# Kernel optimization log

Hardware: AMD Instinct MI355X
Metric: run time of the kernel (lower is better)

## Reference

```python
import jax, jax.numpy as jnp
import numpy as np

D_MODEL = 1024
N_HEAD = 16
D_K = D_MODEL // N_HEAD


def setup_inputs() -> dict:
    key = jax.random.key(0)
    ks = jax.random.split(key, 7)
    B, S = 4, 2048
    scale = 1.0 / np.sqrt(D_MODEL)
    x = jax.random.normal(ks[0], (B, S, D_MODEL), dtype=jnp.float32)
    Wq = jax.random.normal(ks[1], (D_MODEL, D_MODEL), dtype=jnp.float32) * scale
    Wk = jax.random.normal(ks[2], (D_MODEL, D_MODEL), dtype=jnp.float32) * scale
    Wv = jax.random.normal(ks[3], (D_MODEL, D_MODEL), dtype=jnp.float32) * scale
    bq = jax.random.normal(ks[4], (D_MODEL,), dtype=jnp.float32) * 0.01
    bk = jax.random.normal(ks[5], (D_MODEL,), dtype=jnp.float32) * 0.01
    bv = jax.random.normal(ks[6], (D_MODEL,), dtype=jnp.float32) * 0.01
    return {"x": x, "Wq": Wq, "bq": bq, "Wk": Wk, "bk": bk, "Wv": Wv, "bv": bv}


def reference(x, Wq, bq, Wk, bk, Wv, bv):
    B, S, _ = x.shape
    # QKV projections (nn.Linear: x @ W.T + b; weights here stored as [in, out])
    Q = x @ Wq + bq  # [B, S, D]
    K = x @ Wk + bk
    V = x @ Wv + bv
    # split heads -> [B, H, S, d_k]
    def split(t):
        return t.reshape(B, S, N_HEAD, D_K).transpose(0, 2, 1, 3)
    Qh, Kh, Vh = split(Q), split(K), split(V)
    scores = jnp.einsum('bhqd,bhkd->bhqk', Qh, Kh) / jnp.sqrt(jnp.float32(D_K))
    attn = jax.nn.softmax(scores, axis=-1)
    ctx = jnp.einsum('bhqk,bhkd->bhqd', attn, Vh)  # [B, H, S, d_k]
    return ctx.transpose(0, 2, 1, 3).reshape(B, S, D_MODEL)
```

## Files before the change

### kernel.cpp

```cpp
#include <hip/hip_runtime.h>
#include <stdint.h>

#define D_MODEL 1024
#define NHEAD   16
#define DK      64
#define BATCH   4
#define SEQ     2048
#define MTOT    (BATCH*SEQ)
#define KVB     64
#define NT      (SEQ/KVB)

typedef __attribute__((ext_vector_type(4)))  float  f32x4;
typedef __attribute__((ext_vector_type(16))) float  f32x16;
typedef __attribute__((ext_vector_type(8)))  __bf16 bf16x8;
typedef __attribute__((ext_vector_type(8)))  unsigned short u16x8;
typedef __attribute__((ext_vector_type(4)))  unsigned int u32x4;

#define QSCALE 0.1803368801111244f

__device__ __forceinline__ unsigned short f2bf(float f) {
    unsigned u = __builtin_bit_cast(unsigned, f);
    u += 0x7fffu + ((u >> 16) & 1u);
    return (unsigned short)(u >> 16);
}

__global__ __launch_bounds__(256) void cvt_x_kernel(const float* __restrict__ x,
                                                    unsigned short* __restrict__ xb) {
    size_t i = ((size_t)blockIdx.x * 256 + threadIdx.x) * 8;
    f32x4 a = *(const f32x4*)(x + i);
    f32x4 b = *(const f32x4*)(x + i + 4);
    u16x8 o;
    o[0] = f2bf(a[0]); o[1] = f2bf(a[1]); o[2] = f2bf(a[2]); o[3] = f2bf(a[3]);
    o[4] = f2bf(b[0]); o[5] = f2bf(b[1]); o[6] = f2bf(b[2]); o[7] = f2bf(b[3]);
    *(u16x8*)(xb + i) = o;
}

__global__ __launch_bounds__(256) void cvt_wt_kernel(const float* __restrict__ Wq,
                                                     const float* __restrict__ Wk,
                                                     const float* __restrict__ Wv,
                                                     unsigned short* __restrict__ wt) {
    __shared__ float tile[32][33];
    int mat = blockIdx.z;
    const float* W = (mat == 0) ? Wq : (mat == 1) ? Wk : Wv;
    int n0 = blockIdx.x * 32;
    int k0 = blockIdx.y * 32;
    int tx = threadIdx.x;
    int ty = threadIdx.y;
    #pragma unroll
    for (int i = 0; i < 4; ++i)
        tile[ty + i*8][tx] = W[(size_t)(k0 + ty + i*8) * D_MODEL + n0 + tx];
    __syncthreads();
    unsigned short* dst = wt + (size_t)mat * D_MODEL * D_MODEL;
    #pragma unroll
    for (int i = 0; i < 4; ++i)
        dst[(size_t)(n0 + ty + i*8) * D_MODEL + k0 + tx] = f2bf(tile[tx][ty + i*8]);
}

#define BM 128
#define BN 128
#define BKK 64
__global__ __launch_bounds__(256) void qkv_gemm_kernel(const unsigned short* __restrict__ xb,
                                                       const unsigned short* __restrict__ wt,
                                                       const float* __restrict__ bq,
                                                       const float* __restrict__ bk,
                                                       const float* __restrict__ bv,
                                                       unsigned short* __restrict__ qkv) {
    __shared__ __align__(16) unsigned char sA[BM * BKK * 2];
    __shared__ __align__(16) unsigned char sB[BN * BKK * 2];

    int nb   = blockIdx.x;
    int mb   = blockIdx.y;
    int mat  = nb >> 3;
    int col0 = (nb & 7) * BN;
    int m0   = mb * BM;
    int t    = threadIdx.x;
    int lane = t & 63;
    int w    = t >> 6;

    const unsigned short* wmat = wt + (size_t)mat * D_MODEL * D_MODEL;
    const float* bias = (mat == 0) ? bq : (mat == 1) ? bk : bv;

    f32x4 acc[4][4];
    #pragma unroll
    for (int i = 0; i < 4; ++i)
        #pragma unroll
        for (int j = 0; j < 4; ++j)
            acc[i][j] = (f32x4)0.0f;

    int rA = (w >> 1) * 64;
    int rB = (w & 1) * 64;

    for (int ks = 0; ks < D_MODEL / BKK; ++ks) {
        int K0 = ks * BKK;
        #pragma unroll
        for (int i = 0; i < 4; ++i) {
            int c   = t + 256 * i;
            int row = c >> 3;
            int kc  = c & 7;
            int swz = kc ^ (row & 7);
            const unsigned short* ga = xb + (size_t)(m0 + row) * D_MODEL + K0 + swz * 8;
            __builtin_amdgcn_global_load_lds(
                (const __attribute__((address_space(1))) void*)ga,
                (__attribute__((address_space(3))) void*)(sA + c * 16), 16, 0, 0);
            const unsigned short* gb = wmat + (size_t)(col0 + row) * D_MODEL + K0 + swz * 8;
            __builtin_amdgcn_global_load_lds(
                (const __attribute__((address_space(1))) void*)gb,
                (__attribute__((address_space(3))) void*)(sB + c * 16), 16, 0, 0);
        }
        __syncthreads();

        #pragma unroll
        for (int kk = 0; kk < 2; ++kk) {
            bf16x8 af[4], bf[4];
            int kc = kk * 4 + (lane >> 4);
            #pragma unroll
            for (int mt = 0; mt < 4; ++mt) {
                int row = rA + mt * 16 + (lane & 15);
                int swz = kc ^ (row & 7);
                af[mt] = *(const bf16x8*)(sA + row * 128 + swz * 16);
            }
            #pragma unroll
            for (int nt = 0; nt < 4; ++nt) {
                int row = rB + nt * 16 + (lane & 15);
                int swz = kc ^ (row & 7);
                bf[nt] = *(const bf16x8*)(sB + row * 128 + swz * 16);
            }
            #pragma unroll
            for (int mt = 0; mt < 4; ++mt)
                #pragma unroll
                for (int nt = 0; nt < 4; ++nt)
                    acc[mt][nt] = __builtin_amdgcn_mfma_f32_16x16x32_bf16(
                        af[mt], bf[nt], acc[mt][nt], 0, 0, 0);
        }
        __syncthreads();
    }

    #pragma unroll
    for (int mt = 0; mt < 4; ++mt) {
        #pragma unroll
        for (int nt = 0; nt < 4; ++nt) {
            int gn = col0 + rB + nt * 16 + (lane & 15);
            float bval = bias[gn];
            #pragma unroll
            for (int r = 0; r < 4; ++r) {
                int gm = m0 + rA + mt * 16 + (lane >> 4) * 4 + r;
                float v = acc[mt][nt][r] + bval;
                if (mat == 0) v *= QSCALE;
                int b = gm >> 11, s = gm & 2047;
                int h = gn >> 6,  d = gn & 63;
                size_t idx;
                if (mat == 2)
                    idx = ((size_t)(b * NHEAD + h) * DK + d) * SEQ + s;
                else
                    idx = ((size_t)(b * NHEAD + h) * SEQ + s) * DK + d;
                qkv[(size_t)mat * MTOT * D_MODEL + idx] = f2bf(v);
            }
        }
    }
}

#define CVTPK(dst, lo_, hi_) \
    asm("v_cvt_pk_bf16_f32 %0, %1, %2" : "=v"(dst) : "v"(lo_), "v"(hi_))
#define PLSWAP(x_, y_) \
    asm("v_permlane32_swap_b32 %0, %1" : "+v"(x_), "+v"(y_))
#define EXP2(dst, x_) \
    asm("v_exp_f32 %0, %1" : "=v"(dst) : "v"(x_))

__device__ __forceinline__ bf16x8 make_pf(float p0, float p1, float p2, float p3,
                                          float p4, float p5, float p6, float p7) {
    unsigned a1, a2, b1, b2;
    CVTPK(a1, p0, p1); CVTPK(a2, p2, p3);
    CVTPK(b1, p4, p5); CVTPK(b2, p6, p7);
    PLSWAP(a1, b1); PLSWAP(a2, b2);
    u32x4 u = { a1, a2, b1, b2 };
    return __builtin_bit_cast(bf16x8, u);
}

__device__ __forceinline__ float vmax16(const f32x16& v) {
    float a = fmaxf(fmaxf(v[0], v[1]),   fmaxf(v[2], v[3]));
    float b = fmaxf(fmaxf(v[4], v[5]),   fmaxf(v[6], v[7]));
    float c = fmaxf(fmaxf(v[8], v[9]),   fmaxf(v[10], v[11]));
    float d = fmaxf(fmaxf(v[12], v[13]), fmaxf(v[14], v[15]));
    return fmaxf(fmaxf(a, b), fmaxf(c, d));
}

__global__ __launch_bounds__(512, 2) void attn_kernel(const unsigned short* __restrict__ qkv,
                                                      float* __restrict__ out) {
    __shared__ __align__(16) unsigned char lds[32768];

    int bh = blockIdx.x;
    int qb = blockIdx.y;
    int t = threadIdx.x;
    int lane = t & 63;
    int w = t >> 6;
    int hi = lane >> 5;
    int l31 = lane & 31;

    const unsigned short* Qb = qkv + (size_t)bh * SEQ * DK;
    const unsigned short* Kb = qkv + (size_t)MTOT * D_MODEL + (size_t)bh * SEQ * DK;
    const unsigned short* Vt = qkv + (size_t)2 * MTOT * D_MODEL + (size_t)bh * DK * SEQ;

    int qbase = qb * 256 + w * 32;

    bf16x8 aq[4];
    #pragma unroll
    for (int kd = 0; kd < 4; ++kd)
        aq[kd] = *(const bf16x8*)(Qb + (size_t)(qbase + l31) * DK + kd * 16 + hi * 8);

    f32x16 o0 = (f32x16)0.0f, o1 = (f32x16)0.0f;
    float mrun = -3e38f, lrun = 0.0f;

#define STAGE(tile_, bo_) do {                                                         \
    int kv0_ = (tile_) * KVB;                                                          \
    int row_ = t >> 3, kc_ = t & 7;                                                    \
    int sw_ = (kc_ ^ (row_ & 7)) * 8;                                                  \
    __builtin_amdgcn_global_load_lds(                                                  \
        (const __attribute__((address_space(1))) void*)(Kb + (size_t)(kv0_ + row_) * DK + sw_), \
        (__attribute__((address_space(3))) void*)(lds + (bo_) + t * 16), 16, 0, 0);             \
    __builtin_amdgcn_global_load_lds(                                                  \
        (const __attribute__((address_space(1))) void*)(Vt + (size_t)row_ * SEQ + kv0_ + sw_),  \
        (__attribute__((address_space(3))) void*)(lds + 16384 + (bo_) + t * 16), 16, 0, 0);     \
} while (0)

    int swz7 = l31 & 7;
    int cofs0 = ((0 + hi) ^ swz7) << 4;
    int cofs1 = ((2 + hi) ^ swz7) << 4;
    int cofs2 = ((4 + hi) ^ swz7) << 4;
    int cofs3 = ((6 + hi) ^ swz7) << 4;

    STAGE(0, 0);
    __syncthreads();
    int buf = 0;

    for (int kt = 0; kt < NT; ++kt) {
        if (kt + 1 < NT)
            STAGE(kt + 1, (buf ^ 1) * 8192);

        const unsigned char* kb = lds + buf * 8192;
        const unsigned char* vb = lds + 16384 + buf * 8192;
        const unsigned char* kr0 = kb + l31 * 128;
        const unsigned char* kr1 = kb + (32 + l31) * 128;
        const unsigned char* vr0 = vb + l31 * 128;
        const unsigned char* vr1 = vb + (32 + l31) * 128;

        bf16x8 ak00 = *(const bf16x8*)(kr0 + cofs0);
        bf16x8 ak01 = *(const bf16x8*)(kr0 + cofs1);
        bf16x8 ak02 = *(const bf16x8*)(kr0 + cofs2);
        bf16x8 ak03 = *(const bf16x8*)(kr0 + cofs3);
        bf16x8 ak10 = *(const bf16x8*)(kr1 + cofs0);
        bf16x8 ak11 = *(const bf16x8*)(kr1 + cofs1);
        bf16x8 ak12 = *(const bf16x8*)(kr1 + cofs2);
        bf16x8 ak13 = *(const bf16x8*)(kr1 + cofs3);
        f32x16 sc0 = (f32x16)0.0f, sc1 = (f32x16)0.0f;
        __builtin_amdgcn_s_setprio(1);
        sc0 = __builtin_amdgcn_mfma_f32_32x32x16_bf16(ak00, aq[0], sc0, 0, 0, 0);
        sc1 = __builtin_amdgcn_mfma_f32_32x32x16_bf16(ak10, aq[0], sc1, 0, 0, 0);
        sc0 = __builtin_amdgcn_mfma_f32_32x32x16_bf16(ak01, aq[1], sc0, 0, 0, 0);
        sc1 = __builtin_amdgcn_mfma_f32_32x32x16_bf16(ak11, aq[1], sc1, 0, 0, 0);
        sc0 = __builtin_amdgcn_mfma_f32_32x32x16_bf16(ak02, aq[2], sc0, 0, 0, 0);
        sc1 = __builtin_amdgcn_mfma_f32_32x32x16_bf16(ak12, aq[2], sc1, 0, 0, 0);
        sc0 = __builtin_amdgcn_mfma_f32_32x32x16_bf16(ak03, aq[3], sc0, 0, 0, 0);
        sc1 = __builtin_amdgcn_mfma_f32_32x32x16_bf16(ak13, aq[3], sc1, 0, 0, 0);
        __builtin_amdgcn_s_setprio(0);

        bf16x8 av00 = *(const bf16x8*)(vr0 + cofs0);
        bf16x8 av01 = *(const bf16x8*)(vr0 + cofs1);
        bf16x8 av02 = *(const bf16x8*)(vr0 + cofs2);
        bf16x8 av03 = *(const bf16x8*)(vr0 + cofs3);
        bf16x8 av10 = *(const bf16x8*)(vr1 + cofs0);
        bf16x8 av11 = *(const bf16x8*)(vr1 + cofs1);
        bf16x8 av12 = *(const bf16x8*)(vr1 + cofs2);
        bf16x8 av13 = *(const bf16x8*)(vr1 + cofs3);

        float mx = fmaxf(vmax16(sc0), vmax16(sc1));
        mx = fmaxf(mx, __shfl_xor(mx, 32));
        if (!__all(mx <= mrun + 8.0f)) {
            float mnew = fmaxf(mrun, mx);
            float al;  EXP2(al, mrun - mnew);
            lrun *= al;
            #pragma unroll
            for (int i = 0; i < 16; ++i) { o0[i] *= al; o1[i] *= al; }
            mrun = mnew;
        }
        #pragma unroll
        for (int i = 0; i < 16; ++i) { float p; EXP2(p, sc0[i] - mrun); sc0[i] = p; }
        #pragma unroll
        for (int i = 0; i < 16; ++i) { float p; EXP2(p, sc1[i] - mrun); sc1[i] = p; }
        float r0 = 0.f, r1 = 0.f, r2 = 0.f, r3 = 0.f;
        #pragma unroll
        for (int i = 0; i < 4; ++i) {
            r0 += sc0[i] + sc1[i];     r1 += sc0[4+i] + sc1[4+i];
            r2 += sc0[8+i] + sc1[8+i]; r3 += sc0[12+i] + sc1[12+i];
        }
        float rs = (r0 + r1) + (r2 + r3);
        rs += __shfl_xor(rs, 32);
        lrun += rs;

        bf16x8 pf0 = make_pf(sc0[0], sc0[1], sc0[2],  sc0[3],  sc0[4],  sc0[5],  sc0[6],  sc0[7]);
        bf16x8 pf1 = make_pf(sc0[8], sc0[9], sc0[10], sc0[11], sc0[12], sc0[13], sc0[14], sc0[15]);
        bf16x8 pf2 = make_pf(sc1[0], sc1[1], sc1[2],  sc1[3],  sc1[4],  sc1[5],  sc1[6],  sc1[7]);
        bf16x8 pf3 = make_pf(sc1[8], sc1[9], sc1[10], sc1[11], sc1[12], sc1[13], sc1[14], sc1[15]);

        __builtin_amdgcn_s_setprio(1);
        o0 = __builtin_amdgcn_mfma_f32_32x32x16_bf16(av00, pf0, o0, 0, 0, 0);
        o1 = __builtin_amdgcn_mfma_f32_32x32x16_bf16(av10, pf0, o1, 0, 0, 0);
        o0 = __builtin_amdgcn_mfma_f32_32x32x16_bf16(av01, pf1, o0, 0, 0, 0);
        o1 = __builtin_amdgcn_mfma_f32_32x32x16_bf16(av11, pf1, o1, 0, 0, 0);
        o0 = __builtin_amdgcn_mfma_f32_32x32x16_bf16(av02, pf2, o0, 0, 0, 0);
        o1 = __builtin_amdgcn_mfma_f32_32x32x16_bf16(av12, pf2, o1, 0, 0, 0);
        o0 = __builtin_amdgcn_mfma_f32_32x32x16_bf16(av03, pf3, o0, 0, 0, 0);
        o1 = __builtin_amdgcn_mfma_f32_32x32x16_bf16(av13, pf3, o1, 0, 0, 0);
        __builtin_amdgcn_s_setprio(0);

        __syncthreads();
        buf ^= 1;
    }
#undef STAGE

    int b = bh >> 4, h = bh & 15;
    float rl = 1.0f / lrun;
    float* dst = out + ((size_t)b * SEQ + qbase + l31) * D_MODEL + h * DK;
    #pragma unroll
    for (int g = 0; g < 4; ++g) {
        int d0 = 8 * g + 4 * hi;
        f32x4 v0 = { o0[4*g] * rl, o0[4*g+1] * rl, o0[4*g+2] * rl, o0[4*g+3] * rl };
        *(f32x4*)(dst + d0) = v0;
        f32x4 v1 = { o1[4*g] * rl, o1[4*g+1] * rl, o1[4*g+2] * rl, o1[4*g+3] * rl };
        *(f32x4*)(dst + 32 + d0) = v1;
    }
}

extern "C" void kernel_launch(void* const* d_in, const int* in_sizes, int n_in,
                              void* d_out, int out_size, void* d_ws, size_t ws_size,
                              hipStream_t stream) {
    const float* x  = (const float*)d_in[0];
    const float* Wq = (const float*)d_in[1];
    const float* bq = (const float*)d_in[2];
    const float* Wk = (const float*)d_in[3];
    const float* bk = (const float*)d_in[4];
    const float* Wv = (const float*)d_in[5];
    const float* bv = (const float*)d_in[6];
    float* out = (float*)d_out;

    unsigned short* xb  = (unsigned short*)d_ws;
    unsigned short* wt  = xb + (size_t)MTOT * D_MODEL;
    unsigned short* qkv = wt + (size_t)3 * D_MODEL * D_MODEL;

    cvt_x_kernel<<<dim3(MTOT * D_MODEL / (256 * 8)), dim3(256), 0, stream>>>(x, xb);
    cvt_wt_kernel<<<dim3(32, 32, 3), dim3(32, 8), 0, stream>>>(Wq, Wk, Wv, wt);
    qkv_gemm_kernel<<<dim3(24, 64), dim3(256), 0, stream>>>(xb, wt, bq, bk, bv, qkv);
    attn_kernel<<<dim3(64, 8), dim3(512), 0, stream>>>(qkv, out);
}
```

Before: 201.0 us.

## Triple-buffer attention K/V staging, swizzle GEMM block order, reshape max tree

The attention kernel moves from double to triple buffering of K/V tiles in LDS (48KB). Each iteration prefetches two tiles ahead and waits with explicit vmcnt counts plus a raw barrier, so global load latency can overlap more compute. The QKV GEMM remaps its block index so consecutive blocks are spread across M rows, aiming at better L2 locality. The row-max reduction tree is also restructured. The cost is more LDS per block, which could limit occupancy at two blocks per CU, and the hand-written vmcnt waits are correctness-sensitive.

```diff
diff --git a/kernel.cpp b/kernel.cpp
--- a/kernel.cpp
+++ b/kernel.cpp
@@ -68,8 +68,10 @@
     __shared__ __align__(16) unsigned char sA[BM * BKK * 2];
     __shared__ __align__(16) unsigned char sB[BN * BKK * 2];
 
-    int nb   = blockIdx.x;
-    int mb   = blockIdx.y;
+    int lin = blockIdx.y * 24 + blockIdx.x;
+    lin = (lin & 7) * 192 + (lin >> 3);
+    int nb   = lin % 24;
+    int mb   = lin / 24;
     int mat  = nb >> 3;
     int col0 = (nb & 7) * BN;
     int m0   = mb * BM;
@@ -177,16 +179,18 @@
 }
 
 __device__ __forceinline__ float vmax16(const f32x16& v) {
-    float a = fmaxf(fmaxf(v[0], v[1]),   fmaxf(v[2], v[3]));
-    float b = fmaxf(fmaxf(v[4], v[5]),   fmaxf(v[6], v[7]));
-    float c = fmaxf(fmaxf(v[8], v[9]),   fmaxf(v[10], v[11]));
-    float d = fmaxf(fmaxf(v[12], v[13]), fmaxf(v[14], v[15]));
+    float a = fmaxf(fmaxf(v[0],  v[1]),  v[2]);
+    float b = fmaxf(fmaxf(v[3],  v[4]),  v[5]);
+    float c = fmaxf(fmaxf(v[6],  v[7]),  v[8]);
+    float d = fmaxf(fmaxf(v[9],  v[10]), v[11]);
+    a = fmaxf(fmaxf(a, v[12]), v[13]);
+    b = fmaxf(fmaxf(b, v[14]), v[15]);
     return fmaxf(fmaxf(a, b), fmaxf(c, d));
 }
 
 __global__ __launch_bounds__(512, 2) void attn_kernel(const unsigned short* __restrict__ qkv,
                                                       float* __restrict__ out) {
-    __shared__ __align__(16) unsigned char lds[32768];
+    __shared__ __align__(16) unsigned char lds[49152];
 
     int bh = blockIdx.x;
     int qb = blockIdx.y;
@@ -210,16 +214,16 @@
     f32x16 o0 = (f32x16)0.0f, o1 = (f32x16)0.0f;
     float mrun = -3e38f, lrun = 0.0f;
 
-#define STAGE(tile_, bo_) do {                                                         \
+#define STAGE(tile_, b_) do {                                                          \
     int kv0_ = (tile_) * KVB;                                                          \
     int row_ = t >> 3, kc_ = t & 7;                                                    \
     int sw_ = (kc_ ^ (row_ & 7)) * 8;                                                  \
     __builtin_amdgcn_global_load_lds(                                                  \
         (const __attribute__((address_space(1))) void*)(Kb + (size_t)(kv0_ + row_) * DK + sw_), \
-        (__attribute__((address_space(3))) void*)(lds + (bo_) + t * 16), 16, 0, 0);             \
+        (__attribute__((address_space(3))) void*)(lds + (b_) * 8192 + t * 16), 16, 0, 0);       \
     __builtin_amdgcn_global_load_lds(                                                  \
         (const __attribute__((address_space(1))) void*)(Vt + (size_t)row_ * SEQ + kv0_ + sw_),  \
-        (__attribute__((address_space(3))) void*)(lds + 16384 + (bo_) + t * 16), 16, 0, 0);     \
+        (__attribute__((address_space(3))) void*)(lds + 24576 + (b_) * 8192 + t * 16), 16, 0, 0); \
 } while (0)
 
     int swz7 = l31 & 7;
@@ -229,15 +233,18 @@
     int cofs3 = ((6 + hi) ^ swz7) << 4;
 
     STAGE(0, 0);
-    __syncthreads();
-    int buf = 0;
+    STAGE(1, 1);
+    asm volatile("s_waitcnt vmcnt(2)" ::: "memory");
+    __builtin_amdgcn_s_barrier();
+
+    int b0 = 0, b1 = 1, b2 = 2;
 
     for (int kt = 0; kt < NT; ++kt) {
-        if (kt + 1 < NT)
-            STAGE(kt + 1, (buf ^ 1) * 8192);
-
-        const unsigned char* kb = lds + buf * 8192;
-        const unsigned char* vb = lds + 16384 + buf * 8192;
+        if (kt + 2 < NT)
+            STAGE(kt + 2, b2);
+
+        const unsigned char* kb = lds + b0 * 8192;
+        const unsigned char* vb = lds + 24576 + b0 * 8192;
         const unsigned char* kr0 = kb + l31 * 128;
         const unsigned char* kr1 = kb + (32 + l31) * 128;
         const unsigned char* vr0 = vb + l31 * 128;
@@ -312,8 +319,14 @@
         o1 = __builtin_amdgcn_mfma_f32_32x32x16_bf16(av13, pf3, o1, 0, 0, 0);
         __builtin_amdgcn_s_setprio(0);
 
-        __syncthreads();
-        buf ^= 1;
+        if (kt + 2 < NT) {
+            asm volatile("s_waitcnt vmcnt(2)" ::: "memory");
+            __builtin_amdgcn_s_barrier();
+        } else if (kt + 1 < NT) {
+            asm volatile("s_waitcnt vmcnt(0)" ::: "memory");
+            __builtin_amdgcn_s_barrier();
+        }
+        int tb = b0; b0 = b1; b1 = b2; b2 = tb;
     }
 #undef STAGE
 
```

New measurement: 198.8 us. Within noise of the previous version (-1.1%).
